# Performance work log

Hardware: AMD Instinct MI355X
Metric: run time of the kernel (lower is better)

The kernel has to match this reference:

```python
import jax, jax.numpy as jnp
import numpy as np

K = 512
HIDDEN = 256


def setup_inputs() -> dict:
    key = jax.random.key(0)
    k1, k2 = jax.random.split(key)
    z = jax.random.normal(k1, (8, 8192, HIDDEN), dtype=jnp.float32)
    # codebook init: uniform(-1/k, 1/k) as in the torch module
    codebook = jax.random.uniform(k2, (K, HIDDEN), dtype=jnp.float32,
                                  minval=-1.0 / K, maxval=1.0 / K)
    return {"z": z, "codebook": codebook}


def reference(z, codebook):
    # squared L2 distance to every code, expanded form to avoid the
    # [N, k, hidden] intermediate: ||z||^2 - 2 z.c + ||c||^2
    z2 = jnp.sum(z * z, axis=-1, keepdims=True)            # [B, T, 1]
    c2 = jnp.sum(codebook * codebook, axis=-1)             # [k]
    cross = jnp.einsum('bth,kh->btk', z, codebook)         # [B, T, k]
    distances = z2 - 2.0 * cross + c2                      # [B, T, k]
    ind = jnp.argmin(distances, axis=-1)                   # [B, T] int
    z_q = codebook[ind]                                    # [B, T, hidden]

    vq_loss = jnp.mean((z_q - jax.lax.stop_gradient(z)) ** 2)
    commitment_loss = jnp.mean((z - jax.lax.stop_gradient(z_q)) ** 2)
    z_q_st = z + jax.lax.stop_gradient(z_q - z)
    return (z_q_st, ind, vq_loss + commitment_loss)
```

## Files before the change

### kernel.cpp

```cpp
#include <hip/hip_runtime.h>

#define M_TOKENS 65536
#define HID      256
#define KCODES   512

#define IND_OFF  (M_TOKENS * HID)
#define LOSS_OFF (IND_OFF + M_TOKENS)

#define TAU      1.5e-4f

#define WS_C2_OFF        16
#define WS_BHI_OFF       4096
#define WS_BLO_OFF       (4096 + 262144)
#define WS_LIST_OFF_FAST (4096 + 524288)
#define WS_LIST_OFF_SLOW 4096
#define WS_MIN_FAST      (WS_LIST_OFF_FAST + 8192 * 4)

typedef __attribute__((ext_vector_type(8))) short  short8;
typedef __attribute__((ext_vector_type(4))) float  f32x4;

__device__ inline unsigned short f2bf(float f) {
    unsigned u = __float_as_uint(f);
    u += 0x7FFF + ((u >> 16) & 1);
    return (unsigned short)(u >> 16);
}
__device__ inline float bf2f(unsigned short h) {
    return __uint_as_float(((unsigned)h) << 16);
}

__global__ __launch_bounds__(256) void vq_prep(
    const float* __restrict__ cb,
    unsigned short* __restrict__ Bhi, unsigned short* __restrict__ Blo,
    float* __restrict__ c2, double* __restrict__ acc, int* __restrict__ cnt) {
    int b = blockIdx.x;
    if (b < 64) {
        int g = b * 256 + threadIdx.x;
        int frag = g >> 6, lane = g & 63;
        int nb = frag >> 3, kb = frag & 7;
        int code = nb * 16 + (lane & 15);
        int kk = kb * 32 + (lane >> 4) * 8;
        const float4* s4 = reinterpret_cast<const float4*>(cb + code * HID + kk);
        float4 v0 = s4[0], v1 = s4[1];
        float f[8] = {v0.x, v0.y, v0.z, v0.w, v1.x, v1.y, v1.z, v1.w};
        short8 vh, vl;
        #pragma unroll
        for (int j = 0; j < 8; ++j) {
            unsigned short h = f2bf(f[j]);
            vh[j] = (short)h;
            vl[j] = (short)f2bf(f[j] - bf2f(h));
        }
        *reinterpret_cast<short8*>(Bhi + (size_t)g * 8) = vh;
        *reinterpret_cast<short8*>(Blo + (size_t)g * 8) = vl;
    } else {
        if (b == 64 && threadIdx.x == 0) { *acc = 0.0; *cnt = 0; }
        int k = (b - 64) * 256 + threadIdx.x;
        const float* row = cb + k * HID;
        double s = 0.0;
        for (int i = 0; i < HID; ++i) {
            double v = (double)row[i];
            s = fma(v, v, s);
        }
        c2[k] = (float)s;
    }
}

__global__ __launch_bounds__(256, 2) void vq_main_mfma(
    const float* __restrict__ z, const float* __restrict__ cb,
    const float* __restrict__ c2g,
    const unsigned short* __restrict__ Bhi,
    const unsigned short* __restrict__ Blo,
    float* __restrict__ out, double* __restrict__ loss_acc,
    int* __restrict__ cnt, int* __restrict__ list, int cap) {

    __shared__ short8 ldsB[2][16][64];
    __shared__ float  lds_c2[KCODES];

    const int tid  = threadIdx.x;
    const int wid  = tid >> 6;
    const int lane = tid & 63;
    const int q    = lane >> 4;
    const int tokW = blockIdx.x * 128 + wid * 32;

    const float4* z4  = reinterpret_cast<const float4*>(z);
    const float4* cb4 = reinterpret_cast<const float4*>(cb);

    lds_c2[tid]       = c2g[tid];
    lds_c2[tid + 256] = c2g[tid + 256];

#define STAGE(nbv, bufv) do {                                                  \
        _Pragma("unroll")                                                      \
        for (int j = 0; j < 4; ++j) {                                          \
            int f_  = (wid << 2) | j;                                          \
            int kb_ = f_ & 7;                                                  \
            const unsigned short* src_ =                                       \
                ((f_ < 8) ? Bhi : Blo) +                                       \
                (((size_t)((nbv) * 8 + kb_) * 64 + lane) << 3);                \
            __builtin_amdgcn_global_load_lds(                                  \
                (const __attribute__((address_space(1))) void*)src_,           \
                (__attribute__((address_space(3))) void*)&ldsB[bufv][f_][0],   \
                16, 0, 0);                                                     \
        }                                                                      \
    } while (0)

    short8 ah[2][8], al[2][8];
    float sq[2];
    #pragma unroll
    for (int mf = 0; mf < 2; ++mf) {
        int token = tokW + mf * 16 + (lane & 15);
        const float4* zr = z4 + (size_t)token * 64 + q * 2;
        float s = 0.f;
        #pragma unroll
        for (int kb = 0; kb < 8; ++kb) {
            float4 v0 = zr[kb * 8];
            float4 v1 = zr[kb * 8 + 1];
            float f[8] = {v0.x, v0.y, v0.z, v0.w, v1.x, v1.y, v1.z, v1.w};
            short8 vh, vl;
            #pragma unroll
            for (int j = 0; j < 8; ++j) {
                unsigned short h = f2bf(f[j]);
                vh[j] = (short)h;
                vl[j] = (short)f2bf(f[j] - bf2f(h));
                s = fmaf(f[j], f[j], s);
            }
            ah[mf][kb] = vh;
            al[mf][kb] = vl;
        }
        s += __shfl_xor(s, 16, 64);
        s += __shfl_xor(s, 32, 64);
        sq[mf] = s;
    }

    STAGE(0, 0);
    __syncthreads();

    float b1[2][4], b2[2][4];
    int   i1[2][4];
    #pragma unroll
    for (int mf = 0; mf < 2; ++mf)
        #pragma unroll
        for (int r = 0; r < 4; ++r) { b1[mf][r] = 3.4e38f; b2[mf][r] = 3.4e38f; i1[mf][r] = 0; }

    for (int nb = 0; nb < 32; ++nb) {
        int buf = nb & 1;
        if (nb < 31) STAGE(nb + 1, buf ^ 1);

        f32x4 a0 = {0.f, 0.f, 0.f, 0.f};
        f32x4 a1 = {0.f, 0.f, 0.f, 0.f};
        #pragma unroll
        for (int kb = 0; kb < 8; ++kb) {
            short8 vbh = ldsB[buf][kb][lane];
            short8 vbl = ldsB[buf][8 + kb][lane];
            a0 = __builtin_amdgcn_mfma_f32_16x16x32_bf16(ah[0][kb], vbh, a0, 0, 0, 0);
            a1 = __builtin_amdgcn_mfma_f32_16x16x32_bf16(ah[1][kb], vbh, a1, 0, 0, 0);
            a0 = __builtin_amdgcn_mfma_f32_16x16x32_bf16(al[0][kb], vbh, a0, 0, 0, 0);
            a1 = __builtin_amdgcn_mfma_f32_16x16x32_bf16(al[1][kb], vbh, a1, 0, 0, 0);
            a0 = __builtin_amdgcn_mfma_f32_16x16x32_bf16(ah[0][kb], vbl, a0, 0, 0, 0);
            a1 = __builtin_amdgcn_mfma_f32_16x16x32_bf16(ah[1][kb], vbl, a1, 0, 0, 0);
        }
        int code = nb * 16 + (lane & 15);
        float c2v = lds_c2[code];
        #pragma unroll
        for (int r = 0; r < 4; ++r) {
            float s0 = fmaf(-2.f, a0[r], c2v);
            if (s0 < b1[0][r]) { b2[0][r] = b1[0][r]; b1[0][r] = s0; i1[0][r] = code; }
            else if (s0 < b2[0][r]) b2[0][r] = s0;
            float s1 = fmaf(-2.f, a1[r], c2v);
            if (s1 < b1[1][r]) { b2[1][r] = b1[1][r]; b1[1][r] = s1; i1[1][r] = code; }
            else if (s1 < b2[1][r]) b2[1][r] = s1;
        }
        __syncthreads();
    }
#undef STAGE

    #pragma unroll
    for (int st = 1; st <= 8; st <<= 1) {
        #pragma unroll
        for (int mf = 0; mf < 2; ++mf)
            #pragma unroll
            for (int r = 0; r < 4; ++r) {
                float ob1 = __shfl_xor(b1[mf][r], st, 64);
                int   oi1 = __shfl_xor(i1[mf][r], st, 64);
                float ob2 = __shfl_xor(b2[mf][r], st, 64);
                if (ob1 < b1[mf][r] || (ob1 == b1[mf][r] && oi1 < i1[mf][r])) {
                    b2[mf][r] = fminf(b1[mf][r], ob2);
                    b1[mf][r] = ob1;
                    i1[mf][r] = oi1;
                } else {
                    b2[mf][r] = fminf(b2[mf][r], ob1);
                }
            }
    }

    if ((lane & 15) == 0) {
        #pragma unroll
        for (int mf = 0; mf < 2; ++mf) {
            float4 iv;
            #pragma unroll
            for (int r = 0; r < 4; ++r) {
                ((float*)&iv)[r] = (float)i1[mf][r];
                if (b2[mf][r] - b1[mf][r] <= TAU) {
                    int pos = atomicAdd(cnt, 1);
                    if (pos < cap) list[pos] = tokW + mf * 16 + q * 4 + r;
                }
            }
            *reinterpret_cast<float4*>(out + IND_OFF + tokW + mf * 16 + q * 4) = iv;
        }
    }

    double lsum = 0.0;
    #pragma unroll
    for (int mf = 0; mf < 2; ++mf)
        #pragma unroll
        for (int r = 0; r < 4; ++r) {
            float z2r = __shfl(sq[mf], (lane & 48) | (q * 4 + r), 64);
            if ((lane & 15) == 0) lsum += (double)z2r + (double)b1[mf][r];
        }
    lsum += __shfl_xor(lsum, 16, 64);
    lsum += __shfl_xor(lsum, 32, 64);
    if (lane == 0) atomicAdd(loss_acc, lsum);

    float4* out4 = reinterpret_cast<float4*>(out);
    #pragma unroll
    for (int tt = 0; tt < 32; ++tt) {
        int code = __shfl(i1[tt >> 4][tt & 3], ((tt >> 2) & 3) * 16, 64);
        float4 cv = cb4[(size_t)code * 64 + lane];
        out4[(size_t)(tokW + tt) * 64 + lane] = cv;
    }
}

#define BM   128
#define NC   128
#define KS   32
#define PAD  33

__global__ void vq_init(const float* __restrict__ cb, float* __restrict__ c2,
                        double* __restrict__ acc, int* __restrict__ cnt) {
    int k = threadIdx.x;
    if (k == 0) { *acc = 0.0; *cnt = 0; }
    const float* row = cb + k * HID;
    double s = 0.0;
    for (int i = 0; i < HID; ++i) {
        double v = (double)row[i];
        s = fma(v, v, s);
    }
    c2[k] = (float)s;
}

__global__ __launch_bounds__(256, 2) void vq_main_f32(
    const float* __restrict__ z, const float* __restrict__ cb,
    const float* __restrict__ c2g, float* __restrict__ out,
    double* __restrict__ loss_acc, int* __restrict__ cnt,
    int* __restrict__ list, int cap) {

    __shared__ float smem[(BM + NC) * PAD];
    float* zs = smem;
    float* cs = smem + BM * PAD;

    const int tid = threadIdx.x;
    const int tx = tid & 15;
    const int ty = tid >> 4;
    const int tokBase = blockIdx.x * BM;

    const float4* z4g  = reinterpret_cast<const float4*>(z);
    const float4* cb4g = reinterpret_cast<const float4*>(cb);

    float bs[8], bs2[8];
    int   bi[8];
    #pragma unroll
    for (int m = 0; m < 8; ++m) { bs[m] = 3.4e38f; bs2[m] = 3.4e38f; bi[m] = 0; }

    for (int chunk = 0; chunk < KCODES / NC; ++chunk) {
        float acc[8][8];
        #pragma unroll
        for (int m = 0; m < 8; ++m)
            #pragma unroll
            for (int n = 0; n < 8; ++n) acc[m][n] = 0.f;

        for (int ks = 0; ks < HID / KS; ++ks) {
            __syncthreads();
            #pragma unroll
            for (int i = 0; i < 4; ++i) {
                int f   = tid + i * 256;
                int row = f >> 3;
                int k4  = f & 7;
                float4 zv = z4g[(tokBase + row) * (HID / 4) + ks * (KS / 4) + k4];
                int b = row * PAD + k4 * 4;
                zs[b + 0] = zv.x; zs[b + 1] = zv.y; zs[b + 2] = zv.z; zs[b + 3] = zv.w;
                float4 cv = cb4g[(chunk * NC + row) * (HID / 4) + ks * (KS / 4) + k4];
                cs[b + 0] = cv.x; cs[b + 1] = cv.y; cs[b + 2] = cv.z; cs[b + 3] = cv.w;
            }
            __syncthreads();

            #pragma unroll 2
            for (int k = 0; k < KS; ++k) {
                float zf[8], cf[8];
                #pragma unroll
                for (int m = 0; m < 8; ++m) zf[m] = zs[(ty * 8 + m) * PAD + k];
                #pragma unroll
                for (int n = 0; n < 8; ++n) cf[n] = cs[(tx * 8 + n) * PAD + k];
                #pragma unroll
                for (int m = 0; m < 8; ++m)
                    #pragma unroll
                    for (int n = 0; n < 8; ++n)
                        acc[m][n] = fmaf(zf[m], cf[n], acc[m][n]);
            }
        }

        #pragma unroll
        for (int n = 0; n < 8; ++n) {
            int code = chunk * NC + tx * 8 + n;
            float c2v = c2g[code];
            #pragma unroll
            for (int m = 0; m < 8; ++m) {
                float s = fmaf(-2.f, acc[m][n], c2v);
                if (s < bs[m]) { bs2[m] = bs[m]; bs[m] = s; bi[m] = code; }
                else if (s < bs2[m]) bs2[m] = s;
            }
        }
    }

    __syncthreads();
    float* rs   = smem;
    int*   ri   = reinterpret_cast<int*>(smem + BM * 16);
    float* rs2  = smem + BM * 32;
    int*   inds = reinterpret_cast<int*>(smem + BM * 48);
    float* wred = smem + BM * 48 + BM;

    #pragma unroll
    for (int m = 0; m < 8; ++m) {
        int tok = ty * 8 + m;
        rs [tok * 16 + tx] = bs[m];
        ri [tok * 16 + tx] = bi[m];
        rs2[tok * 16 + tx] = bs2[m];
    }
    __syncthreads();

    if (tid < BM) {
        float B1 = rs[tid * 16];
        int   I1 = ri[tid * 16];
        float B2 = rs2[tid * 16];
        for (int j = 1; j < 16; ++j) {
            float b1v = rs [tid * 16 + j];
            int   i1v = ri [tid * 16 + j];
            float b2v = rs2[tid * 16 + j];
            if (b1v < B1 || (b1v == B1 && i1v < I1)) {
                B2 = fminf(B1, b2v); B1 = b1v; I1 = i1v;
            } else {
                B2 = fminf(B2, b1v);
            }
        }
        inds[tid] = I1;
        out[IND_OFF + tokBase + tid] = (float)I1;
        if (B2 - B1 <= TAU) {
            int pos = atomicAdd(cnt, 1);
            if (pos < cap) list[pos] = tokBase + tid;
        }
    }
    __syncthreads();

    float loc = 0.f;
    float4* out4 = reinterpret_cast<float4*>(out);
    for (int it = 0; it < (BM * HID / 4) / 256; ++it) {
        int e4  = it * 256 + tid;
        int tok = e4 >> 6;
        int h4  = e4 & 63;
        int code = inds[tok];
        float4 cv = cb4g[code * 64 + h4];
        float4 zv = z4g[(tokBase + tok) * 64 + h4];
        out4[(tokBase + tok) * 64 + h4] = cv;
        float dx = cv.x - zv.x, dy = cv.y - zv.y;
        float dz = cv.z - zv.z, dw = cv.w - zv.w;
        loc = fmaf(dx, dx, loc);
        loc = fmaf(dy, dy, loc);
        loc = fmaf(dz, dz, loc);
        loc = fmaf(dw, dw, loc);
    }
    #pragma unroll
    for (int off = 32; off > 0; off >>= 1) loc += __shfl_xor(loc, off, 64);
    int wave = tid >> 6;
    if ((tid & 63) == 0) wred[wave] = loc;
    __syncthreads();
    if (tid == 0) {
        double t = (double)wred[0] + (double)wred[1] +
                   (double)wred[2] + (double)wred[3];
        atomicAdd(loss_acc, t);
    }
}

__global__ __launch_bounds__(256) void vq_refine(
    const float* __restrict__ z, const float* __restrict__ cb,
    const float* __restrict__ c2g, const double* __restrict__ loss_acc,
    const int* __restrict__ cnt, const int* __restrict__ list,
    float* __restrict__ out, int cap) {

    if (blockIdx.x == 0 && threadIdx.x == 0)
        out[LOSS_OFF] = (float)(2.0 * (*loss_acc) / (double)(M_TOKENS * HID));

    __shared__ float  zrow[HID];
    __shared__ double red_d[256];
    __shared__ int    red_i[256];

    const int tid = threadIdx.x;
    int n = *cnt; if (n > cap) n = cap;

    for (int idx = blockIdx.x; idx < n; idx += gridDim.x) {
        int t = list[idx];
        float zi = z[t * HID + tid];
        zrow[tid] = zi;
        red_d[tid] = (double)zi * (double)zi;
        __syncthreads();
        for (int s = 128; s > 0; s >>= 1) {
            if (tid < s) red_d[tid] += red_d[tid + s];
            __syncthreads();
        }
        float z2f = (float)red_d[0];
        __syncthreads();

        double bestD = 1e300; int bestK = 1 << 30;
        #pragma unroll
        for (int c = 0; c < 2; ++c) {
            int k = tid + c * 256;
            const float* cr = cb + k * HID;
            double acc = 0.0;
            for (int i = 0; i < HID; ++i)
                acc = fma((double)zrow[i], (double)cr[i], acc);
            float cross32 = (float)acc;
            float u = 2.0f * cross32;
            float tq = (float)((double)z2f - (double)u);
            double v = (double)tq + (double)c2g[k];
            float D = (float)v;
            double Dd = (double)D;
            if (Dd < bestD || (Dd == bestD && k < bestK)) { bestD = Dd; bestK = k; }
        }
        red_d[tid] = bestD; red_i[tid] = bestK;
        __syncthreads();
        for (int s = 128; s > 0; s >>= 1) {
            if (tid < s) {
                double d2 = red_d[tid + s]; int i2 = red_i[tid + s];
                if (d2 < red_d[tid] || (d2 == red_d[tid] && i2 < red_i[tid])) {
                    red_d[tid] = d2; red_i[tid] = i2;
                }
            }
            __syncthreads();
        }
        int best = red_i[0];
        if (tid == 0) out[IND_OFF + t] = (float)best;
        out[t * HID + tid] = cb[best * HID + tid];
        __syncthreads();
    }
}

extern "C" void kernel_launch(void* const* d_in, const int* in_sizes, int n_in,
                              void* d_out, int out_size, void* d_ws, size_t ws_size,
                              hipStream_t stream) {
    const float* z  = (const float*)d_in[0];
    const float* cb = (const float*)d_in[1];
    float* out = (float*)d_out;
    double* acc = (double*)d_ws;
    int*  cnt = (int*)((char*)d_ws + 8);
    float* c2 = (float*)((char*)d_ws + WS_C2_OFF);

    if (ws_size >= WS_MIN_FAST) {
        unsigned short* Bhi = (unsigned short*)((char*)d_ws + WS_BHI_OFF);
        unsigned short* Blo = (unsigned short*)((char*)d_ws + WS_BLO_OFF);
        int* list = (int*)((char*)d_ws + WS_LIST_OFF_FAST);
        int cap = 8192;
        vq_prep<<<66, 256, 0, stream>>>(cb, Bhi, Blo, c2, acc, cnt);
        vq_main_mfma<<<M_TOKENS / 128, 256, 0, stream>>>(
            z, cb, c2, Bhi, Blo, out, acc, cnt, list, cap);
        vq_refine<<<512, 256, 0, stream>>>(z, cb, c2, acc, cnt, list, out, cap);
    } else {
        int* list = (int*)((char*)d_ws + WS_LIST_OFF_SLOW);
        int cap = 0;
        if (ws_size > WS_LIST_OFF_SLOW + 16) {
            size_t avail = (ws_size - WS_LIST_OFF_SLOW) / 4;
            cap = (avail > 8192) ? 8192 : (int)avail;
        }
        vq_init<<<1, 512, 0, stream>>>(cb, c2, acc, cnt);
        vq_main_f32<<<M_TOKENS / BM, 256, 0, stream>>>(
            z, cb, c2, out, acc, cnt, list, cap);
        vq_refine<<<512, 256, 0, stream>>>(z, cb, c2, acc, cnt, list, out, cap);
    }
}
```

Before: 175.4 us.

## Triple-buffer codebook LDS staging and vectorize slow-path double dot products

The main MFMA loop moves from a double-buffered LDS staging scheme with two __syncthreads per iteration to a triple-buffered ring. It prefetches two blocks ahead and uses a single barrier guarded by an explicit vmcnt wait, which is meant to hide global-load latency and cut synchronisation. Separately, the fallback exact-recompute kernel now computes both code dot products in one pass with float4 loads and eight independent double accumulators. That shortens the FMA dependency chain and reduces scalar loads. Costs are more LDS per block (which may limit occupancy), hand-tuned waitcnt values that must match STAGE's load count, a wasted final prefetch, and a changed summation order in the fallback that could alter rounding at tie-breaks.

Measured after the change: 181.0 us. 3.2% more time.

```diff
diff --git a/kernel.cpp b/kernel.cpp
--- a/kernel.cpp
+++ b/kernel.cpp
@@ -72,7 +72,7 @@
     float* __restrict__ out, double* __restrict__ loss_acc,
     int* __restrict__ cnt, int* __restrict__ list, int cap) {
 
-    __shared__ short8 ldsB[2][16][64];
+    __shared__ short8 ldsB[3][16][64];
     __shared__ float  lds_c2[KCODES];
 
     const int tid  = threadIdx.x;
@@ -131,7 +131,8 @@
     }
 
     STAGE(0, 0);
-    __syncthreads();
+    STAGE(1, 1);
+    asm volatile("s_waitcnt lgkmcnt(0)" ::: "memory");
 
     float b1[2][4], b2[2][4];
     int   i1[2][4];
@@ -140,16 +141,20 @@
         #pragma unroll
         for (int r = 0; r < 4; ++r) { b1[mf][r] = 3.4e38f; b2[mf][r] = 3.4e38f; i1[mf][r] = 0; }
 
+    int bcur = 0, bnx2 = 2;
     for (int nb = 0; nb < 32; ++nb) {
-        int buf = nb & 1;
-        if (nb < 31) STAGE(nb + 1, buf ^ 1);
+        asm volatile("s_waitcnt vmcnt(4)" ::: "memory");
+        __builtin_amdgcn_s_barrier();
+        __builtin_amdgcn_sched_barrier(0);
+
+        STAGE((nb + 2) & 31, bnx2);
 
         f32x4 a0 = {0.f, 0.f, 0.f, 0.f};
         f32x4 a1 = {0.f, 0.f, 0.f, 0.f};
         #pragma unroll
         for (int kb = 0; kb < 8; ++kb) {
-            short8 vbh = ldsB[buf][kb][lane];
-            short8 vbl = ldsB[buf][8 + kb][lane];
+            short8 vbh = ldsB[bcur][kb][lane];
+            short8 vbl = ldsB[bcur][8 + kb][lane];
             a0 = __builtin_amdgcn_mfma_f32_16x16x32_bf16(ah[0][kb], vbh, a0, 0, 0, 0);
             a1 = __builtin_amdgcn_mfma_f32_16x16x32_bf16(ah[1][kb], vbh, a1, 0, 0, 0);
             a0 = __builtin_amdgcn_mfma_f32_16x16x32_bf16(al[0][kb], vbh, a0, 0, 0, 0);
@@ -168,7 +173,8 @@
             if (s1 < b1[1][r]) { b2[1][r] = b1[1][r]; b1[1][r] = s1; i1[1][r] = code; }
             else if (s1 < b2[1][r]) b2[1][r] = s1;
         }
-        __syncthreads();
+        bcur = (bcur == 2) ? 0 : bcur + 1;
+        bnx2 = (bnx2 == 2) ? 0 : bnx2 + 1;
     }
 #undef STAGE
 
@@ -416,15 +422,32 @@
         float z2f = (float)red_d[0];
         __syncthreads();
 
+        const float4* zr4 = reinterpret_cast<const float4*>(zrow);
+        const float4* c0  = reinterpret_cast<const float4*>(cb + tid * HID);
+        const float4* c1  = reinterpret_cast<const float4*>(cb + (tid + 256) * HID);
+        double p00 = 0, p01 = 0, p02 = 0, p03 = 0;
+        double p10 = 0, p11 = 0, p12 = 0, p13 = 0;
+        #pragma unroll 4
+        for (int i = 0; i < HID / 4; ++i) {
+            float4 zv = zr4[i];
+            float4 a = c0[i];
+            float4 b = c1[i];
+            p00 = fma((double)zv.x, (double)a.x, p00);
+            p01 = fma((double)zv.y, (double)a.y, p01);
+            p02 = fma((double)zv.z, (double)a.z, p02);
+            p03 = fma((double)zv.w, (double)a.w, p03);
+            p10 = fma((double)zv.x, (double)b.x, p10);
+            p11 = fma((double)zv.y, (double)b.y, p11);
+            p12 = fma((double)zv.z, (double)b.z, p12);
+            p13 = fma((double)zv.w, (double)b.w, p13);
+        }
         double bestD = 1e300; int bestK = 1 << 30;
         #pragma unroll
         for (int c = 0; c < 2; ++c) {
             int k = tid + c * 256;
-            const float* cr = cb + k * HID;
-            double acc = 0.0;
-            for (int i = 0; i < HID; ++i)
-                acc = fma((double)zrow[i], (double)cr[i], acc);
-            float cross32 = (float)acc;
+            double accd = (c == 0) ? ((p00 + p01) + (p02 + p03))
+                                   : ((p10 + p11) + (p12 + p13));
+            float cross32 = (float)accd;
             float u = 2.0f * cross32;
             float tq = (float)((double)z2f - (double)u);
             double v = (double)tq + (double)c2g[k];
```
